# Kernel optimization log

Hardware: AMD Instinct MI355X
Metric: run time of the kernel (lower is better)

## Reference

```python
import jax, jax.numpy as jnp
import numpy as np

T, NC, NT, D, H, LBL = 8, 512, 512, 256, 8, 3
NBF = 1419  # performer default: int(256 * ln(256))
EPS = 1e-4


def setup_inputs() -> dict:
    key = jax.random.key(0)
    ks = jax.random.split(key, 16)
    rn = lambda i, shape, sc=1.0: jax.random.normal(ks[i], shape, dtype=jnp.float32) * sc
    w = 1.0 / np.sqrt(D)
    return {
        'x_ctx': rn(0, (T, NC, D)),
        'label_train': rn(1, (T, NC, LBL)),
        'x_tgt': rn(2, (T, NT, D)),
        # task_encoder: 3-layer MLP (256+label_dim -> 256 -> 256 -> 256), ReLU
        'W1': rn(3, (D + LBL, D), 1.0 / np.sqrt(D + LBL)), 'b1': jnp.zeros((D,), jnp.float32),
        'W2': rn(4, (D, D), w), 'b2': jnp.zeros((D,), jnp.float32),
        'W3': rn(5, (D, D), w), 'b3': jnp.zeros((D,), jnp.float32),
        # per-head projections (8 distinct 256->256 Linears each for k/v/q)
        'Wk': rn(6, (H, D, D), w), 'bk': jnp.zeros((H, D), jnp.float32),
        'Wv': rn(7, (H, D, D), w), 'bv': jnp.zeros((H, D), jnp.float32),
        'Wq': rn(8, (H, D, D), w), 'bq': jnp.zeros((H, D), jnp.float32),
        # output head-merge projection (8*256 -> 256) and mu (256 -> 256)
        'Wo': rn(9, (H * D, D), 1.0 / np.sqrt(H * D)), 'bo': jnp.zeros((D,), jnp.float32),
        'Wmu': rn(10, (D, D), w), 'bmu': jnp.zeros((D,), jnp.float32),
        # FAVOR+ random projection matrix [nb_features, dim_head]
        'proj': rn(11, (NBF, D)),
    }


def _softmax_kernel(data, proj, is_query):
    # Performer FAVOR+ positive softmax-kernel features. data: [t,h,n,d]
    dn = D ** -0.25
    ratio = NBF ** -0.5
    dd = jnp.einsum('thnd,fd->thnf', data * dn, proj)          # [t,h,n,F]
    diag = 0.5 * jnp.sum(data * data, axis=-1) * (dn * dn)      # [t,h,n]
    if is_query:
        m = jnp.max(dd, axis=-1, keepdims=True)
    else:
        m = jnp.max(dd, axis=(-2, -1), keepdims=True)
    return ratio * (jnp.exp(dd - diag[..., None] - m) + EPS)


def reference(x_ctx, label_train, x_tgt, W1, b1, W2, b2, W3, b3,
              Wk, bk, Wv, bv, Wq, bq, Wo, bo, Wmu, bmu, proj):
    # task_encoder MLP on [x_ctx, label]
    h = jax.nn.relu(jnp.concatenate([x_ctx, label_train], axis=-1) @ W1 + b1)
    h = jax.nn.relu(h @ W2 + b2)
    cf = jax.nn.relu(h @ W3 + b3)                               # context_features [t,Nc,D]
    # per-head full-width projections: k from x_ctx, v from context_features, q from x_tgt
    k = jnp.einsum('tnd,hde->thne', x_ctx, Wk) + bk[None, :, None, :]
    v = jnp.einsum('tnd,hde->thne', cf, Wv) + bv[None, :, None, :]
    q = jnp.einsum('tnd,hde->thne', x_tgt, Wq) + bq[None, :, None, :]
    # non-causal Performer linear attention
    qp = _softmax_kernel(q, proj, True)                         # [t,h,Nt,F]
    kp = _softmax_kernel(k, proj, False)                        # [t,h,Nc,F]
    ksum = jnp.sum(kp, axis=-2)                                 # [t,h,F]
    d_inv = 1.0 / jnp.einsum('thnf,thf->thn', qp, ksum)         # [t,h,Nt]
    ctx = jnp.einsum('thnf,thne->thfe', kp, v)                  # [t,h,F,D]
    out = jnp.einsum('thnf,thfe,thn->thne', qp, ctx, d_inv)     # [t,h,Nt,D]
    # torch: permute(0,2,3,1).view(t,Nt,-1) -> head index fastest-varying
    out = jnp.transpose(out, (0, 2, 3, 1)).reshape(out.shape[0], out.shape[2], -1)
    rep = out @ Wo + bo                                         # [t,Nt,D]
    return rep @ Wmu + bmu                                      # mu / sample_features
```

## Files before the change

### kernel.cpp

```cpp
#include <hip/hip_runtime.h>
#include <hip/hip_bf16.h>

typedef __hip_bfloat16 bf16;
typedef __attribute__((ext_vector_type(8))) short short8;
typedef __attribute__((ext_vector_type(4))) float f32x4;
typedef __attribute__((ext_vector_type(4))) unsigned short us4;
#define DEV __device__ __forceinline__

static constexpr int T_ = 8, NC = 512, NT = 512, D_ = 256, H_ = 8, NBF = 1419;
static constexpr int FT32 = 46;
static constexpr float EPS_ = 1e-4f;
static constexpr float DN = 0.25f;
static constexpr float DIAG_SC = 0.03125f;

DEV float bf2f(unsigned short u) { return __uint_as_float(((unsigned)u) << 16); }
DEV float tofloat(bf16 x) { return __bfloat162float(x); }
DEV unsigned short f2bu(float x) { bf16 h = __float2bfloat16(x); return *(unsigned short*)&h; }

DEV float ldx(const void* p, long i, int isb) {
  if (isb) return bf2f(((const unsigned short*)p)[i]);
  return ((const float*)p)[i];
}
DEV void stx(void* p, long i, float v, int isb) {
  if (isb) ((bf16*)p)[i] = __float2bfloat16(v);
  else     ((float*)p)[i] = v;
}
DEV void unpack8(uint4 u, float* dst) {
  unsigned w[4] = {u.x, u.y, u.z, u.w};
#pragma unroll
  for (int i = 0; i < 4; i++) {
    dst[2 * i + 0] = __uint_as_float((w[i] & 0xffffu) << 16);
    dst[2 * i + 1] = __uint_as_float(w[i] & 0xffff0000u);
  }
}

DEV void async_copy16(const void* g, void* lds) {
  __builtin_amdgcn_global_load_lds(
      (const __attribute__((address_space(1))) unsigned int*)g,
      (__attribute__((address_space(3))) unsigned int*)lds, 16, 0, 0);
}

__global__ __launch_bounds__(256)
void detect_dtype(const void* __restrict__ x, int* __restrict__ flag)
{
  __shared__ int bad;
  if (threadIdx.x == 0) bad = 0;
  __syncthreads();
  int mybad = 0;
  for (int j = 0; j < 16; j++) {
    long i = 2L * (threadIdx.x + 256L * j);
    unsigned short u = ((const unsigned short*)x)[i];
    int e = (u >> 7) & 0xff, mant = u & 0x7f;
    bool b = (e == 0xff) || (e >= 141) || (e <= 93 && !(e == 0 && mant == 0));
    mybad += b ? 1 : 0;
  }
  atomicAdd(&bad, mybad);
  __syncthreads();
  if (threadIdx.x == 0) *flag = (bad > 1024) ? 0 : 1;
}

__global__ __launch_bounds__(256)
void conv_proj(const void* __restrict__ proj, bf16* __restrict__ projB,
               const int* __restrict__ dtFlag)
{
  const int fl = *dtFlag;
  int f = blockIdx.x, t = threadIdx.x;
  float v = (f < NBF) ? ldx(proj, (long)f * 256 + t, fl) : 0.f;
  projB[(long)f * 256 + t] = __float2bfloat16(v);
}

__global__ __launch_bounds__(256)
void conv_bf16(const void* __restrict__ src, bf16* __restrict__ dst,
               const int* __restrict__ dtFlag)
{
  const int fl = *dtFlag;
  long i = (long)blockIdx.x * 256 + threadIdx.x;
  dst[i] = __float2bfloat16(ldx(src, i, fl));
}

__global__ __launch_bounds__(256)
void conv_wT(const void* __restrict__ Wk, const void* __restrict__ Wv,
             const void* __restrict__ Wq, const void* __restrict__ Wo,
             const void* __restrict__ W1, const void* __restrict__ W2,
             const void* __restrict__ W3, const void* __restrict__ Wmu,
             bf16* __restrict__ WkT, bf16* __restrict__ WvT,
             bf16* __restrict__ WqT, bf16* __restrict__ WoT,
             bf16* __restrict__ W1T, bf16* __restrict__ W2T,
             bf16* __restrict__ W3T, bf16* __restrict__ WmuT,
             const int* __restrict__ dtFlag)
{
  __shared__ float tile[32][33];
  const int fl = *dtFlag;
  const int kt = blockIdx.x, nt = blockIdx.y, z = blockIdx.z, t = threadIdx.x;
  const void* in; bf16* out; int K; int perm = 0; long off = 0;
  if (z < 8)        { in = Wk;  out = WkT;  K = 256; off = (long)z * 65536; }
  else if (z < 16)  { in = Wv;  out = WvT;  K = 256; off = (long)(z - 8) * 65536; }
  else if (z < 24)  { in = Wq;  out = WqT;  K = 256; off = (long)(z - 16) * 65536; }
  else if (z == 24) { in = Wo;  out = WoT;  K = 2048; perm = 1; }
  else if (z == 25) { in = W1;  out = W1T;  K = 256; }
  else if (z == 26) { in = W2;  out = W2T;  K = 256; }
  else if (z == 27) { in = W3;  out = W3T;  K = 256; }
  else              { in = Wmu; out = WmuT; K = 256; }
  if (K == 256 && kt >= 8) return;
  const int k0 = kt * 32, n0 = nt * 32;
  const int row = t >> 3, cb = (t & 7) * 4;
  {
    int kk = k0 + row;
    int krow = perm ? (((kk & 255) << 3) | (kk >> 8)) : kk;
#pragma unroll
    for (int j = 0; j < 4; j++)
      tile[row][cb + j] = ldx(in, off + (long)krow * 256 + n0 + cb + j, fl);
  }
  __syncthreads();
  us4 o;
#pragma unroll
  for (int j = 0; j < 4; j++) o[j] = f2bu(tile[cb + j][row]);
  *(us4*)(out + off + (long)(n0 + row) * K + k0 + cb) = o;
}

__global__ __launch_bounds__(256)
void init_zero(float* __restrict__ p)
{
  p[blockIdx.x * 256 + threadIdx.x] = 0.f;
}

__global__ __launch_bounds__(256)
void gemm_mfma(const bf16* __restrict__ A, const bf16* __restrict__ BT,
               const void* __restrict__ bias,
               void* __restrict__ C, int cMode, int epi, int cT,
               const int* __restrict__ dtFlag, float* __restrict__ diagOut,
               float* __restrict__ svOut,
               int M, int N, int K, long sA, int divA, long sB, int modB, long sBias)
{
  __shared__ alignas(16) bf16 As[2][64 * 64];
  __shared__ alignas(16) bf16 Bs[2][64 * 64];
  const int fl = *dtFlag;
  const int cB = (cMode == 2) ? fl : cMode;
  const int t = threadIdx.x;
  const int bz = blockIdx.z;
  const long aOff = (long)(bz / divA) * sA;
  const long bOff = (long)(bz % modB) * sB;
  const long biasOff = (long)(bz % modB) * sBias;
  const long cOff = (long)bz * (long)M * N;
  const int m0 = blockIdx.y * 64, n0 = blockIdx.x * 64;
  const int w = t >> 6, l = t & 63, quad = l >> 4, ln = l & 15;
  const bf16* Ab = A + aOff + (long)m0 * K;
  const bf16* Bb = BT + bOff + (long)n0 * K;
  const int srow = l >> 3;
  const int scc = (l & 7) ^ srow;
  f32x4 acc[4] = {};

  auto stage = [&](int buf, int k0) {
#pragma unroll
    for (int j = 0; j < 2; j++) {
      const int rbase = 32 * j + 8 * w;
      const int row = rbase + srow;
      async_copy16(Ab + (long)row * K + k0 + scc * 8, &As[buf][rbase * 64]);
      async_copy16(Bb + (long)row * K + k0 + scc * 8, &Bs[buf][rbase * 64]);
    }
  };

  stage(0, 0);
  __syncthreads();

  int cur = 0;
  for (int k0 = 0; k0 < K; k0 += 64) {
    if (k0 + 64 < K) stage(cur ^ 1, k0 + 64);
    const bf16* Ac = &As[cur][0];
    const bf16* Bc = &Bs[cur][0];
    const int arow = 16 * w + ln;
#pragma unroll
    for (int ks = 0; ks < 2; ks++) {
      short8 a = *(const short8*)(Ac + arow * 64 + (((ks * 4 + quad) ^ (arow & 7)) << 3));
#pragma unroll
      for (int i = 0; i < 4; i++) {
        const int brow = 16 * i + ln;
        short8 b = *(const short8*)(Bc + brow * 64 + (((ks * 4 + quad) ^ (brow & 7)) << 3));
        acc[i] = __builtin_amdgcn_mfma_f32_16x16x32_bf16(a, b, acc[i], 0, 0, 0);
      }
    }
    asm volatile("s_waitcnt vmcnt(0)" ::: "memory");
    __builtin_amdgcn_s_barrier();
    __builtin_amdgcn_sched_barrier(0);
    cur ^= 1;
  }

  float s2[4] = {0.f, 0.f, 0.f, 0.f};
  if (cT == 2) {
    const int mm = m0 + 16 * w + quad * 4;
    const int tile = mm >> 5, off = mm & 31;
#pragma unroll
    for (int i = 0; i < 4; i++) {
      int n = n0 + 16 * i + ln;
      us4 cv;
      float colsum = 0.f;
#pragma unroll
      for (int r = 0; r < 4; r++) {
        float c = acc[i][r];
        if (epi >= 1) c += ldx(bias, biasOff + n, fl);
        if (epi == 2) c = fmaxf(c, 0.f);
        colsum += c;
        cv[r] = f2bu(c);
      }
      *(us4*)((bf16*)C + cOff + ((long)tile * N + n) * 32 + off) = cv;
      if (svOut) {
        colsum += __shfl_xor(colsum, 16);
        colsum += __shfl_xor(colsum, 32);
        if (quad == 0) atomicAdd(&svOut[(long)bz * N + n], colsum);
      }
    }
  } else {
#pragma unroll
    for (int i = 0; i < 4; i++) {
#pragma unroll
      for (int r = 0; r < 4; r++) {
        int m = m0 + 16 * w + quad * 4 + r;
        int n = n0 + 16 * i + ln;
        float c = acc[i][r];
        if (epi >= 1) c += ldx(bias, biasOff + n, fl);
        if (epi == 2) c = fmaxf(c, 0.f);
        s2[r] += c * c;
        stx(C, cOff + (long)m * N + n, c, cB);
      }
    }
  }
  if (diagOut) {
#pragma unroll
    for (int r = 0; r < 4; r++) {
      float s = s2[r];
      s += __shfl_xor(s, 1); s += __shfl_xor(s, 2);
      s += __shfl_xor(s, 4); s += __shfl_xor(s, 8);
      if (ln == 0)
        atomicAdd(&diagOut[(long)bz * M + m0 + 16 * w + quad * 4 + r], DIAG_SC * s);
    }
  }
}

__global__ __launch_bounds__(256)
void gemm_wo_splitk(const bf16* __restrict__ A, const bf16* __restrict__ BT,
                    float* __restrict__ P, int M, int N, int K)
{
  __shared__ alignas(16) bf16 As[2][64 * 64];
  __shared__ alignas(16) bf16 Bs[2][64 * 64];
  const int t = threadIdx.x;
  const int z = blockIdx.z;
  const int m0 = blockIdx.y * 64, n0 = blockIdx.x * 64;
  const int w = t >> 6, l = t & 63, quad = l >> 4, ln = l & 15;
  const bf16* Ab = A + (long)m0 * K;
  const bf16* Bb = BT + (long)n0 * K;
  const int srow = l >> 3, scc = (l & 7) ^ srow;
  f32x4 acc[4] = {};
  const int kbase = z * 256, kend = kbase + 256;

  auto stage = [&](int buf, int k0) {
#pragma unroll
    for (int j = 0; j < 2; j++) {
      const int rbase = 32 * j + 8 * w;
      const int row = rbase + srow;
      async_copy16(Ab + (long)row * K + k0 + scc * 8, &As[buf][rbase * 64]);
      async_copy16(Bb + (long)row * K + k0 + scc * 8, &Bs[buf][rbase * 64]);
    }
  };

  stage(0, kbase);
  __syncthreads();

  int cur = 0;
  for (int k0 = kbase; k0 < kend; k0 += 64) {
    if (k0 + 64 < kend) stage(cur ^ 1, k0 + 64);
    const bf16* Ac = &As[cur][0];
    const bf16* Bc = &Bs[cur][0];
    const int arow = 16 * w + ln;
#pragma unroll
    for (int ks = 0; ks < 2; ks++) {
      short8 a = *(const short8*)(Ac + arow * 64 + (((ks * 4 + quad) ^ (arow & 7)) << 3));
#pragma unroll
      for (int i = 0; i < 4; i++) {
        const int brow = 16 * i + ln;
        short8 b = *(const short8*)(Bc + brow * 64 + (((ks * 4 + quad) ^ (brow & 7)) << 3));
        acc[i] = __builtin_amdgcn_mfma_f32_16x16x32_bf16(a, b, acc[i], 0, 0, 0);
      }
    }
    asm volatile("s_waitcnt vmcnt(0)" ::: "memory");
    __builtin_amdgcn_s_barrier();
    __builtin_amdgcn_sched_barrier(0);
    cur ^= 1;
  }

  float* Pz = P + (long)z * M * N;
#pragma unroll
  for (int i = 0; i < 4; i++) {
#pragma unroll
    for (int r = 0; r < 4; r++) {
      int m = m0 + 16 * w + quad * 4 + r;
      int n = n0 + 16 * i + ln;
      Pz[(long)m * N + n] = acc[i][r];
    }
  }
}

__global__ __launch_bounds__(256)
void reduce_partials(const float* __restrict__ P, const void* __restrict__ bo,
                     bf16* __restrict__ rep, const int* __restrict__ dtFlag)
{
  const int fl = *dtFlag;
  long idx = (long)blockIdx.x * 256 + threadIdx.x;
  int n = idx & 255;
  float s = ldx(bo, n, fl);
#pragma unroll
  for (int z = 0; z < 8; z++) s += P[(long)z * 1048576 + idx];
  rep[idx] = __float2bfloat16(s);
}

__global__ __launch_bounds__(256)
void fixup_h1(bf16* __restrict__ h1, const void* __restrict__ label,
              const void* __restrict__ W1, const void* __restrict__ b1,
              const int* __restrict__ dtFlag)
{
  const int fl = *dtFlag;
  int idx = blockIdx.x * 256 + threadIdx.x;
  int m = idx >> 8, n = idx & 255;
  float c = tofloat(h1[idx]) + ldx(b1, n, fl);
#pragma unroll
  for (int j = 0; j < 3; j++)
    c += ldx(label, m * 3 + j, fl) * ldx(W1, (256 + j) * 256 + n, fl);
  h1[idx] = __float2bfloat16(fmaxf(c, 0.f));
}

__global__ __launch_bounds__(256)
void key_fused_mfma(const bf16* __restrict__ k, const bf16* __restrict__ vQ,
                    const bf16* __restrict__ projB, const float* __restrict__ diagk,
                    float* __restrict__ ksumE, bf16* __restrict__ ctxQ,
                    float* __restrict__ mpart)
{
  __shared__ alignas(16) bf16 kS[3][32 * 256];
  __shared__ alignas(16) bf16 pS[2][64 * 40];
  __shared__ float wredM[4];

  const int bz = blockIdx.x, ft = blockIdx.y, f0 = ft * 64;
  const int t = threadIdx.x;
  const int w = t >> 6, l = t & 63, quad = l >> 4, ln = l & 15;
  const int fmine = f0 + 16 * w + ln;
  const bool fv = fmine < NBF;

  const bf16* kb = k + (long)bz * NC * 256;
  const bf16* vqb = vQ + (long)bz * 16 * 256 * 32;
  const float* db = diagk + bz * NC;

  auto stage = [&](int buf, int n0) {
#pragma unroll
    for (int j = 0; j < 4; j++) {
      int row = w * 8 + j * 2 + (l >> 5);
      int cc = (l & 31) ^ ((2 * j + (l >> 5)) & 7);
      async_copy16(kb + (long)(n0 + row) * 256 + cc * 8,
                   &kS[buf][w * 2048 + j * 512]);
    }
  };
  stage(0, 0);
  stage(1, 32);

  short8 pf[8];
  {
    const bf16* prow = projB + (long)fmine * 256;
#pragma unroll
    for (int kc = 0; kc < 8; kc++)
      pf[kc] = *(const short8*)(prow + kc * 32 + quad * 8);
  }

  f32x4 acc[4][4] = {};
  float ksumP = 0.f, mP = -1e30f;

  __syncthreads();

  int cur = 0;
  for (int it = 0; it < 16; it++) {
    const int n0 = it * 32;
    short8 bfr[4];
#pragma unroll
    for (int ei = 0; ei < 4; ei++) {
      int e = 64 * w + 16 * ei + ln;
      bfr[ei] = *(const short8*)(vqb + ((long)it * 256 + e) * 32 + quad * 8);
    }
    f32x4 dv0 = *(const f32x4*)(db + n0 + quad * 4);
    f32x4 dv1 = *(const f32x4*)(db + n0 + 16 + quad * 4);
    __builtin_amdgcn_sched_barrier(0);
    if (it + 2 < 16) {
      int nb = cur + 2; if (nb >= 3) nb -= 3;
      stage(nb, n0 + 64);
    }
    __builtin_amdgcn_sched_barrier(0);

    const bf16* kcur = &kS[cur][0];
    f32x4 dd[2][2] = {};
    __builtin_amdgcn_s_setprio(1);
#pragma unroll
    for (int kc = 0; kc < 8; kc++) {
      const int hf = kc & 1;
#pragma unroll
      for (int mi = 0; mi < 2; mi++) {
        short8 a = *(const short8*)(kcur + (16 * mi + ln) * 256 +
                                    (((kc * 4 + quad) ^ (ln & 7)) << 3));
        dd[mi][hf] = __builtin_amdgcn_mfma_f32_16x16x32_bf16(a, pf[kc], dd[mi][hf], 0, 0, 0);
      }
    }
    __builtin_amdgcn_s_setprio(0);
    bf16* pcur = &pS[it & 1][0];
#pragma unroll
    for (int mi = 0; mi < 2; mi++) {
      us4 ev;
      f32x4 dvv = mi ? dv1 : dv0;
#pragma unroll
      for (int r = 0; r < 4; r++) {
        float sc = DN * (dd[mi][0][r] + dd[mi][1][r]);
        float E = fv ? __expf(fminf(sc - dvv[r], 80.f)) : 0.f;
        unsigned short u = f2bu(E);
        ksumP += bf2f(u);
        if (fv) mP = fmaxf(mP, sc);
        ev[r] = u;
      }
      *(us4*)(pcur + (16 * w + ln) * 40 + 16 * mi + quad * 4) = ev;
    }
    asm volatile("s_waitcnt vmcnt(4) lgkmcnt(0)" ::: "memory");
    __builtin_amdgcn_s_barrier();
    __builtin_amdgcn_sched_barrier(0);

    __builtin_amdgcn_s_setprio(1);
#pragma unroll
    for (int fh = 0; fh < 4; fh++) {
      short8 a = *(const short8*)(pcur + (16 * fh + ln) * 40 + quad * 8);
#pragma unroll
      for (int ei = 0; ei < 4; ei++)
        acc[fh][ei] = __builtin_amdgcn_mfma_f32_16x16x32_bf16(a, bfr[ei], acc[fh][ei], 0, 0, 0);
    }
    __builtin_amdgcn_s_setprio(0);
    cur = (cur == 2) ? 0 : cur + 1;
  }
  __syncthreads();

#pragma unroll
  for (int fh = 0; fh < 4; fh++) {
    const int ft32 = 2 * ft + (fh >> 1);
    const int f32b = 16 * (fh & 1) + quad * 4;
#pragma unroll
    for (int ei = 0; ei < 4; ei++) {
      int e = 64 * w + 16 * ei + ln;
      us4 cv;
#pragma unroll
      for (int r = 0; r < 4; r++) cv[r] = f2bu(acc[fh][ei][r]);
      *(us4*)(&ctxQ[((long)(bz * FT32 + ft32) * 256 + e) * 32 + f32b]) = cv;
    }
  }

  float s = ksumP;
  s += __shfl_xor(s, 16); s += __shfl_xor(s, 32);
  if (quad == 0 && fv) ksumE[(long)bz * NBF + fmine] = s;
  float m = mP;
#pragma unroll
  for (int off = 1; off < 64; off <<= 1) m = fmaxf(m, __shfl_xor(m, off));
  if (l == 0) wredM[w] = m;
  __syncthreads();
  if (t == 0)
    mpart[bz * 23 + ft] = fmaxf(fmaxf(wredM[0], wredM[1]), fmaxf(wredM[2], wredM[3]));
}

__global__ __launch_bounds__(64)
void mk_reduce(const float* __restrict__ mpart, float* __restrict__ mk)
{
  int bz = blockIdx.x, l = threadIdx.x;
  float m = (l < 23) ? mpart[bz * 23 + l] : -1e30f;
#pragma unroll
  for (int off = 32; off > 0; off >>= 1) m = fmaxf(m, __shfl_down(m, off));
  if (l == 0) mk[bz] = m;
}

__global__ __launch_bounds__(256)
void ctx_finQ(bf16* __restrict__ ctxQ, const float* __restrict__ Sv,
              const float* __restrict__ mk, float* __restrict__ ctxs)
{
  int ft32 = blockIdx.x, bz = blockIdx.y, e = threadIdx.x;
  float emk = __expf(-mk[bz]);
  float sve = EPS_ * Sv[bz * 256 + e];
  uint4* row = (uint4*)(ctxQ + ((long)(bz * FT32 + ft32) * 256 + e) * 32);
  int fbase = 32 * ft32;
  float rsum = 0.f;
#pragma unroll
  for (int cchunk = 0; cchunk < 4; cchunk++) {
    float tmp[8];
    unpack8(row[cchunk], tmp);
    unsigned short out[8];
#pragma unroll
    for (int j = 0; j < 8; j++) {
      int f = fbase + cchunk * 8 + j;
      float val = (f < NBF) ? (emk * tmp[j] + sve) : 0.f;
      rsum += val;
      out[j] = f2bu(val);
    }
    row[cchunk] = *(const uint4*)out;
  }
  atomicAdd(&ctxs[bz * 256 + e], rsum);
}

__global__ __launch_bounds__(256)
void ksum_fin(float* __restrict__ ksumE, const float* __restrict__ mk,
              float* __restrict__ ksumtot)
{
  __shared__ float red[4];
  int bz = blockIdx.x, t = threadIdx.x;
  int f = blockIdx.y * 256 + t;
  float emk = __expf(-mk[bz]);
  float s = 0.f;
  if (f < NBF) {
    float kf = emk * ksumE[(long)bz * NBF + f] + (float)NC * EPS_;
    ksumE[(long)bz * NBF + f] = kf;
    s = kf;
  }
#pragma unroll
  for (int off = 32; off > 0; off >>= 1) s += __shfl_down(s, off);
  if ((t & 63) == 0) red[t >> 6] = s;
  __syncthreads();
  if (t == 0) atomicAdd(&ksumtot[bz], red[0] + red[1] + red[2] + red[3]);
}

__global__ __launch_bounds__(256)
void q_fused_mfma(const bf16* __restrict__ q, const bf16* __restrict__ projB,
                  const float* __restrict__ diagq, const bf16* __restrict__ ctxQ,
                  const float* __restrict__ ksum, const float* __restrict__ ctxsum,
                  const float* __restrict__ ksumtot, bf16* __restrict__ merged)
{
  __shared__ alignas(16) bf16 projS[2][32 * 256];
  __shared__ alignas(16) bf16 eS[64 * 40];
  __shared__ float dS[64];
  __shared__ float csS[256];
  __shared__ float sS[64];
  __shared__ float mS[64];

  const int bz = blockIdx.x, nt = blockIdx.y, t = threadIdx.x;
  const int w = t >> 6, l = t & 63, quad = l >> 4, ln = l & 15;
  const int tq = bz / H_, hh = bz % H_;
  const bf16* cqb = ctxQ + (long)bz * FT32 * 256 * 32;
  const bf16* qb = q + ((long)bz * NT + nt * 64) * 256;

  auto stage_proj = [&](int buf, int f0n) {
#pragma unroll
    for (int j = 0; j < 4; j++) {
      int row = 8 * w + 2 * j + (l >> 5);
      int cc = (l & 31) ^ (row & 7);
      async_copy16(projB + (long)(f0n + row) * 256 + cc * 8,
                   &projS[buf][(8 * w + 2 * j) * 256]);
    }
  };
  stage_proj(0, 0);

  short8 qf[8];
  {
    const bf16* qrow = qb + (long)(16 * w + ln) * 256;
#pragma unroll
    for (int kc = 0; kc < 8; kc++)
      qf[kc] = *(const short8*)(qrow + kc * 32 + quad * 8);
  }
  if (t < 64) dS[t] = diagq[(long)bz * NT + nt * 64 + t];
  csS[t] = ctxsum[bz * 256 + t];

  f32x4 acc[4][4] = {};
  float sPart[4] = {0.f, 0.f, 0.f, 0.f};
  float mPart[4] = {0.f, 0.f, 0.f, 0.f};
  __syncthreads();

  for (int ft = 0; ft < FT32; ft++) {
    const int f0 = ft * 32;
    const bf16* pcur = &projS[ft & 1][0];
    short8 cfr[4];
#pragma unroll
    for (int i = 0; i < 4; i++) {
      int e = 16 * (4 * w + i) + ln;
      cfr[i] = *(const short8*)(cqb + ((long)ft * 256 + e) * 32 + quad * 8);
    }
    const float kv0 = (f0 + ln < NBF) ? ksum[(long)bz * NBF + f0 + ln] : 0.f;
    const float kv1 = (f0 + 16 + ln < NBF) ? ksum[(long)bz * NBF + f0 + 16 + ln] : 0.f;
    if (ft + 1 < FT32) stage_proj((ft + 1) & 1, f0 + 32);

    f32x4 dd0 = {}, dd1 = {};
#pragma unroll
    for (int kc = 0; kc < 8; kc++) {
      const int co = ((kc * 4 + quad) ^ (ln & 7)) << 3;
      short8 b0 = *(const short8*)(pcur + ln * 256 + co);
      dd0 = __builtin_amdgcn_mfma_f32_16x16x32_bf16(qf[kc], b0, dd0, 0, 0, 0);
      short8 b1 = *(const short8*)(pcur + (16 + ln) * 256 + co);
      dd1 = __builtin_amdgcn_mfma_f32_16x16x32_bf16(qf[kc], b1, dd1, 0, 0, 0);
    }
    const bool fv0 = (f0 + ln) < NBF;
    const bool fv1 = (f0 + 16 + ln) < NBF;
#pragma unroll
    for (int r = 0; r < 4; r++) {
      float E0 = fv0 ? __expf(fminf(DN * dd0[r], 80.f)) : 0.f;
      float E1 = fv1 ? __expf(fminf(DN * dd1[r], 80.f)) : 0.f;
      bf16 h0 = __float2bfloat16(E0), h1v = __float2bfloat16(E1);
      float e0 = tofloat(h0), e1 = tofloat(h1v);
      eS[(16 * w + quad * 4 + r) * 40 + ln] = h0;
      eS[(16 * w + quad * 4 + r) * 40 + 16 + ln] = h1v;
      sPart[r] += e0 * kv0 + e1 * kv1;
      mPart[r] = fmaxf(mPart[r], fmaxf(e0, e1));
    }
    asm volatile("s_waitcnt lgkmcnt(0)" ::: "memory");
    __builtin_amdgcn_s_barrier();
    __builtin_amdgcn_sched_barrier(0);

#pragma unroll
    for (int mh = 0; mh < 4; mh++) {
      short8 a = *(const short8*)(&eS[(16 * mh + ln) * 40 + quad * 8]);
#pragma unroll
      for (int i = 0; i < 4; i++)
        acc[mh][i] = __builtin_amdgcn_mfma_f32_16x16x32_bf16(a, cfr[i], acc[mh][i], 0, 0, 0);
    }
    asm volatile("s_waitcnt vmcnt(0) lgkmcnt(0)" ::: "memory");
    __builtin_amdgcn_s_barrier();
    __builtin_amdgcn_sched_barrier(0);
  }
  __syncthreads();

#pragma unroll
  for (int r = 0; r < 4; r++) {
    float s = sPart[r], m = mPart[r];
#pragma unroll
    for (int off = 1; off < 16; off <<= 1) {
      s += __shfl_xor(s, off);
      m = fmaxf(m, __shfl_xor(m, off));
    }
    if (ln == 0) {
      sS[16 * w + quad * 4 + r] = s;
      mS[16 * w + quad * 4 + r] = m;
    }
  }
  __syncthreads();

  const float ktotv = ksumtot[bz];
#pragma unroll
  for (int mh = 0; mh < 4; mh++) {
#pragma unroll
    for (int r = 0; r < 4; r++) {
      int row = 16 * mh + quad * 4 + r;
      float st = sS[row];
      float mt = fmaxf(mS[row], 1e-30f);
      float c = __expf(-dS[row]) / mt;
      float inv = 1.f / (c * st + EPS_ * ktotv);
#pragma unroll
      for (int i = 0; i < 4; i++) {
        int e = 16 * (4 * w + i) + ln;
        float val = (c * acc[mh][i][r] + EPS_ * csS[e]) * inv;
        merged[((long)tq * NT + nt * 64 + row) * 2048 + hh * 256 + e] =
            __float2bfloat16(val);
      }
    }
  }
}

extern "C" void kernel_launch(void* const* d_in, const int* in_sizes, int n_in,
                              void* d_out, int out_size, void* d_ws, size_t ws_size,
                              hipStream_t stream)
{
  const void* x_ctx = d_in[0];
  const void* label = d_in[1];
  const void* x_tgt = d_in[2];
  const void* W1 = d_in[3];
  const void* b1 = d_in[4];
  const void* W2 = d_in[5];
  const void* b2 = d_in[6];
  const void* W3 = d_in[7];
  const void* b3 = d_in[8];
  const void* Wk = d_in[9];
  const void* bk = d_in[10];
  const void* Wv = d_in[11];
  const void* bv = d_in[12];
  const void* Wq = d_in[13];
  const void* bq = d_in[14];
  const void* Wo = d_in[15];
  const void* bo = d_in[16];
  const void* Wmu = d_in[17];
  const void* bmu = d_in[18];
  const void* proj = d_in[19];

  float* W = (float*)d_ws;
  const long F0 = 0, F1 = 4194304, F2 = 8388608;
  const long CTXQ_F = (long)64 * FT32 * 256 * 32 / 2;
  const long F3 = F2 + CTXQ_F;
  bf16* kB = (bf16*)(W + F0);
  bf16* qB = (bf16*)(W + F0);
  bf16* rep = (bf16*)(W + F0);
  bf16* vQ = (bf16*)(W + F1);
  bf16* merged = (bf16*)(W + F1);
  bf16* xtB = (bf16*)(W + F1);
  bf16* h1 = (bf16*)(W + F2);
  bf16* h2 = (bf16*)(W + F2 + 524288);
  bf16* cf = (bf16*)(W + F2 + 1048576);
  bf16* xcB = (bf16*)(W + F2 + 1572864);
  bf16* ctxQ = (bf16*)(W + F2);
  float* woP = W + F2;
  long o = F3;
  auto alloc = [&](long n) { float* p = W + o; o += n; return p; };
  float* zbase = W + o;
  float* dgk = alloc(32768);
  float* dgq = alloc(32768);
  float* Sv = alloc(64 * 256);
  float* ctxs = alloc(64 * 256);
  float* ktot = alloc(64);
  alloc(192);
  float* ksumE = alloc((long)64 * NBF);
  float* mpart = alloc(64 * 23);
  float* mk = alloc(64);
  int* dtFlag = (int*)alloc(64);
  bf16* projB = (bf16*)alloc((long)FT32 * 32 * 256 / 2);
  bf16* WkT = (bf16*)alloc(262144);
  bf16* WvT = (bf16*)alloc(262144);
  bf16* WqT = (bf16*)alloc(262144);
  bf16* WoT = (bf16*)alloc(262144);
  bf16* W1T = (bf16*)alloc(32768);
  bf16* W2T = (bf16*)alloc(32768);
  bf16* W3T = (bf16*)alloc(32768);
  bf16* WmuT = (bf16*)alloc(32768);
  (void)ws_size; (void)in_sizes; (void)n_in; (void)out_size;

  const dim3 B(256);
  detect_dtype<<<1, B, 0, stream>>>(x_ctx, dtFlag);
  conv_proj<<<FT32 * 32, B, 0, stream>>>(proj, projB, dtFlag);
  conv_wT<<<dim3(64, 8, 29), B, 0, stream>>>(Wk, Wv, Wq, Wo, W1, W2, W3, Wmu,
                                             WkT, WvT, WqT, WoT, W1T, W2T, W3T, WmuT, dtFlag);
  conv_bf16<<<4096, B, 0, stream>>>(x_ctx, xcB, dtFlag);
  init_zero<<<385, B, 0, stream>>>(zbase);
  gemm_mfma<<<dim3(4, 64, 1), B, 0, stream>>>(
      xcB, W1T, nullptr, h1, 1, 0, 0, dtFlag, nullptr, nullptr,
      4096, 256, 256, 0L, 1, 0L, 1, 0L);
  fixup_h1<<<4096, B, 0, stream>>>(h1, label, W1, b1, dtFlag);
  gemm_mfma<<<dim3(4, 64, 1), B, 0, stream>>>(
      h1, W2T, b2, h2, 1, 2, 0, dtFlag, nullptr, nullptr,
      4096, 256, 256, 0L, 1, 0L, 1, 0L);
  gemm_mfma<<<dim3(4, 64, 1), B, 0, stream>>>(
      h2, W3T, b3, cf, 1, 2, 0, dtFlag, nullptr, nullptr,
      4096, 256, 256, 0L, 1, 0L, 1, 0L);
  gemm_mfma<<<dim3(4, 8, 64), B, 0, stream>>>(
      xcB, WkT, bk, kB, 1, 1, 0, dtFlag, dgk, nullptr,
      512, 256, 256, 131072L, 8, 65536L, 8, 256L);
  gemm_mfma<<<dim3(4, 8, 64), B, 0, stream>>>(
      cf, WvT, bv, vQ, 1, 1, 2, dtFlag, nullptr, Sv,
      512, 256, 256, 131072L, 8, 65536L, 8, 256L);
  key_fused_mfma<<<dim3(64, 23), B, 0, stream>>>(kB, vQ, projB, dgk, ksumE, ctxQ, mpart);
  mk_reduce<<<64, 64, 0, stream>>>(mpart, mk);
  ctx_finQ<<<dim3(FT32, 64), B, 0, stream>>>(ctxQ, Sv, mk, ctxs);
  ksum_fin<<<dim3(64, 6), B, 0, stream>>>(ksumE, mk, ktot);
  conv_bf16<<<4096, B, 0, stream>>>(x_tgt, xtB, dtFlag);
  gemm_mfma<<<dim3(4, 8, 64), B, 0, stream>>>(
      xtB, WqT, bq, qB, 1, 1, 0, dtFlag, dgq, nullptr,
      512, 256, 256, 131072L, 8, 65536L, 8, 256L);
  q_fused_mfma<<<dim3(64, 8), B, 0, stream>>>(qB, projB, dgq, ctxQ, ksumE, ctxs, ktot, merged);
  gemm_wo_splitk<<<dim3(4, 64, 8), B, 0, stream>>>(merged, WoT, woP, 4096, 256, 2048);
  reduce_partials<<<4096, B, 0, stream>>>(woP, bo, rep, dtFlag);
  gemm_mfma<<<dim3(4, 64, 1), B, 0, stream>>>(
      rep, WmuT, bmu, d_out, 2, 1, 0, dtFlag, nullptr, nullptr,
      4096, 256, 256, 0L, 1, 0L, 1, 0L);
}
```

Baseline: 425.1 us.

## Fold key-side max/eps normalization into query kernel; drop ctx_finQ and ksum_fin

The key kernel now also accumulates raw column sums of ctx and the total ksum via atomics. The query kernel applies the exp(-mk) scaling and the EPS terms algebraically in its epilogue, which removes the ctx_finQ and ksum_fin passes that re-read and re-wrote ctxQ and ksumE. It also cuts Wo split-K from 8 to 2 partial slices, so the reduction reads less. In exchange the key kernel's K staging goes from triple to double buffering with a full vmcnt(0) wait, which may expose load latency. The query kernel now reads an un-rescaled ksumE, which relies on the algebra matching exactly.

```diff
diff --git a/kernel.cpp b/kernel.cpp
--- a/kernel.cpp
+++ b/kernel.cpp
@@ -24,14 +24,6 @@
 DEV void stx(void* p, long i, float v, int isb) {
   if (isb) ((bf16*)p)[i] = __float2bfloat16(v);
   else     ((float*)p)[i] = v;
-}
-DEV void unpack8(uint4 u, float* dst) {
-  unsigned w[4] = {u.x, u.y, u.z, u.w};
-#pragma unroll
-  for (int i = 0; i < 4; i++) {
-    dst[2 * i + 0] = __uint_as_float((w[i] & 0xffffu) << 16);
-    dst[2 * i + 1] = __uint_as_float(w[i] & 0xffff0000u);
-  }
 }
 
 DEV void async_copy16(const void* g, void* lds) {
@@ -250,7 +242,7 @@
   const bf16* Bb = BT + (long)n0 * K;
   const int srow = l >> 3, scc = (l & 7) ^ srow;
   f32x4 acc[4] = {};
-  const int kbase = z * 256, kend = kbase + 256;
+  const int kbase = z * 1024, kend = kbase + 1024;
 
   auto stage = [&](int buf, int k0) {
 #pragma unroll
@@ -306,9 +298,7 @@
   const int fl = *dtFlag;
   long idx = (long)blockIdx.x * 256 + threadIdx.x;
   int n = idx & 255;
-  float s = ldx(bo, n, fl);
-#pragma unroll
-  for (int z = 0; z < 8; z++) s += P[(long)z * 1048576 + idx];
+  float s = ldx(bo, n, fl) + P[idx] + P[1048576 + idx];
   rep[idx] = __float2bfloat16(s);
 }
 
@@ -331,9 +321,10 @@
 void key_fused_mfma(const bf16* __restrict__ k, const bf16* __restrict__ vQ,
                     const bf16* __restrict__ projB, const float* __restrict__ diagk,
                     float* __restrict__ ksumE, bf16* __restrict__ ctxQ,
-                    float* __restrict__ mpart)
-{
-  __shared__ alignas(16) bf16 kS[3][32 * 256];
+                    float* __restrict__ mpart, float* __restrict__ csR,
+                    float* __restrict__ ktotR)
+{
+  __shared__ alignas(16) bf16 kS[2][32 * 256];
   __shared__ alignas(16) bf16 pS[2][64 * 40];
   __shared__ float wredM[4];
 
@@ -357,7 +348,6 @@
     }
   };
   stage(0, 0);
-  stage(1, 32);
 
   short8 pf[8];
   {
@@ -384,10 +374,7 @@
     f32x4 dv0 = *(const f32x4*)(db + n0 + quad * 4);
     f32x4 dv1 = *(const f32x4*)(db + n0 + 16 + quad * 4);
     __builtin_amdgcn_sched_barrier(0);
-    if (it + 2 < 16) {
-      int nb = cur + 2; if (nb >= 3) nb -= 3;
-      stage(nb, n0 + 64);
-    }
+    if (it + 1 < 16) stage(cur ^ 1, n0 + 32);
     __builtin_amdgcn_sched_barrier(0);
 
     const bf16* kcur = &kS[cur][0];
@@ -420,7 +407,7 @@
       }
       *(us4*)(pcur + (16 * w + ln) * 40 + 16 * mi + quad * 4) = ev;
     }
-    asm volatile("s_waitcnt vmcnt(4) lgkmcnt(0)" ::: "memory");
+    asm volatile("s_waitcnt vmcnt(0) lgkmcnt(0)" ::: "memory");
     __builtin_amdgcn_s_barrier();
     __builtin_amdgcn_sched_barrier(0);
 
@@ -433,7 +420,7 @@
         acc[fh][ei] = __builtin_amdgcn_mfma_f32_16x16x32_bf16(a, bfr[ei], acc[fh][ei], 0, 0, 0);
     }
     __builtin_amdgcn_s_setprio(0);
-    cur = (cur == 2) ? 0 : cur + 1;
+    cur ^= 1;
   }
   __syncthreads();
 
@@ -451,9 +438,26 @@
     }
   }
 
+#pragma unroll
+  for (int ei = 0; ei < 4; ei++) {
+    float col = 0.f;
+#pragma unroll
+    for (int fh = 0; fh < 4; fh++)
+#pragma unroll
+      for (int r = 0; r < 4; r++) col += acc[fh][ei][r];
+    col += __shfl_xor(col, 16);
+    col += __shfl_xor(col, 32);
+    if (quad == 0) atomicAdd(&csR[(long)bz * 256 + 64 * w + 16 * ei + ln], col);
+  }
+
   float s = ksumP;
   s += __shfl_xor(s, 16); s += __shfl_xor(s, 32);
   if (quad == 0 && fv) ksumE[(long)bz * NBF + fmine] = s;
+  float s2 = s;
+  s2 += __shfl_xor(s2, 1); s2 += __shfl_xor(s2, 2);
+  s2 += __shfl_xor(s2, 4); s2 += __shfl_xor(s2, 8);
+  if (l == 0) atomicAdd(&ktotR[bz], s2);
+
   float m = mP;
 #pragma unroll
   for (int off = 1; off < 64; off <<= 1) m = fmaxf(m, __shfl_xor(m, off));
@@ -474,71 +478,27 @@
 }
 
 __global__ __launch_bounds__(256)
-void ctx_finQ(bf16* __restrict__ ctxQ, const float* __restrict__ Sv,
-              const float* __restrict__ mk, float* __restrict__ ctxs)
-{
-  int ft32 = blockIdx.x, bz = blockIdx.y, e = threadIdx.x;
-  float emk = __expf(-mk[bz]);
-  float sve = EPS_ * Sv[bz * 256 + e];
-  uint4* row = (uint4*)(ctxQ + ((long)(bz * FT32 + ft32) * 256 + e) * 32);
-  int fbase = 32 * ft32;
-  float rsum = 0.f;
-#pragma unroll
-  for (int cchunk = 0; cchunk < 4; cchunk++) {
-    float tmp[8];
-    unpack8(row[cchunk], tmp);
-    unsigned short out[8];
-#pragma unroll
-    for (int j = 0; j < 8; j++) {
-      int f = fbase + cchunk * 8 + j;
-      float val = (f < NBF) ? (emk * tmp[j] + sve) : 0.f;
-      rsum += val;
-      out[j] = f2bu(val);
-    }
-    row[cchunk] = *(const uint4*)out;
-  }
-  atomicAdd(&ctxs[bz * 256 + e], rsum);
-}
-
-__global__ __launch_bounds__(256)
-void ksum_fin(float* __restrict__ ksumE, const float* __restrict__ mk,
-              float* __restrict__ ksumtot)
-{
-  __shared__ float red[4];
-  int bz = blockIdx.x, t = threadIdx.x;
-  int f = blockIdx.y * 256 + t;
-  float emk = __expf(-mk[bz]);
-  float s = 0.f;
-  if (f < NBF) {
-    float kf = emk * ksumE[(long)bz * NBF + f] + (float)NC * EPS_;
-    ksumE[(long)bz * NBF + f] = kf;
-    s = kf;
-  }
-#pragma unroll
-  for (int off = 32; off > 0; off >>= 1) s += __shfl_down(s, off);
-  if ((t & 63) == 0) red[t >> 6] = s;
-  __syncthreads();
-  if (t == 0) atomicAdd(&ksumtot[bz], red[0] + red[1] + red[2] + red[3]);
-}
-
-__global__ __launch_bounds__(256)
 void q_fused_mfma(const bf16* __restrict__ q, const bf16* __restrict__ projB,
                   const float* __restrict__ diagq, const bf16* __restrict__ ctxQ,
-                  const float* __restrict__ ksum, const float* __restrict__ ctxsum,
-                  const float* __restrict__ ksumtot, bf16* __restrict__ merged)
+                  const float* __restrict__ ksum, const float* __restrict__ Sv,
+                  const float* __restrict__ csR, const float* __restrict__ ktotR,
+                  const float* __restrict__ mk, bf16* __restrict__ merged)
 {
   __shared__ alignas(16) bf16 projS[2][32 * 256];
   __shared__ alignas(16) bf16 eS[64 * 40];
   __shared__ float dS[64];
-  __shared__ float csS[256];
+  __shared__ float svS[256];
+  __shared__ float crS[256];
   __shared__ float sS[64];
   __shared__ float mS[64];
+  __shared__ float seS[64];
 
   const int bz = blockIdx.x, nt = blockIdx.y, t = threadIdx.x;
   const int w = t >> 6, l = t & 63, quad = l >> 4, ln = l & 15;
   const int tq = bz / H_, hh = bz % H_;
   const bf16* cqb = ctxQ + (long)bz * FT32 * 256 * 32;
   const bf16* qb = q + ((long)bz * NT + nt * 64) * 256;
+  const float emk = __expf(-mk[bz]);
 
   auto stage_proj = [&](int buf, int f0n) {
 #pragma unroll
@@ -559,10 +519,12 @@
       qf[kc] = *(const short8*)(qrow + kc * 32 + quad * 8);
   }
   if (t < 64) dS[t] = diagq[(long)bz * NT + nt * 64 + t];
-  csS[t] = ctxsum[bz * 256 + t];
+  svS[t] = Sv[bz * 256 + t];
+  crS[t] = csR[bz * 256 + t];
 
   f32x4 acc[4][4] = {};
   float sPart[4] = {0.f, 0.f, 0.f, 0.f};
+  float sEp[4] = {0.f, 0.f, 0.f, 0.f};
   float mPart[4] = {0.f, 0.f, 0.f, 0.f};
   __syncthreads();
 
@@ -599,6 +561,7 @@
       eS[(16 * w + quad * 4 + r) * 40 + ln] = h0;
       eS[(16 * w + quad * 4 + r) * 40 + 16 + ln] = h1v;
       sPart[r] += e0 * kv0 + e1 * kv1;
+      sEp[r] += e0 + e1;
       mPart[r] = fmaxf(mPart[r], fmaxf(e0, e1));
     }
     asm volatile("s_waitcnt lgkmcnt(0)" ::: "memory");
@@ -620,33 +583,38 @@
 
 #pragma unroll
   for (int r = 0; r < 4; r++) {
-    float s = sPart[r], m = mPart[r];
+    float s = sPart[r], m = mPart[r], se = sEp[r];
 #pragma unroll
     for (int off = 1; off < 16; off <<= 1) {
       s += __shfl_xor(s, off);
       m = fmaxf(m, __shfl_xor(m, off));
+      se += __shfl_xor(se, off);
     }
     if (ln == 0) {
       sS[16 * w + quad * 4 + r] = s;
       mS[16 * w + quad * 4 + r] = m;
-    }
-  }
-  __syncthreads();
-
-  const float ktotv = ksumtot[bz];
+      seS[16 * w + quad * 4 + r] = se;
+    }
+  }
+  __syncthreads();
+
+  const float ktotv = ktotR[bz];
 #pragma unroll
   for (int mh = 0; mh < 4; mh++) {
 #pragma unroll
     for (int r = 0; r < 4; r++) {
       int row = 16 * mh + quad * 4 + r;
       float st = sS[row];
+      float se = seS[row];
       float mt = fmaxf(mS[row], 1e-30f);
       float c = __expf(-dS[row]) / mt;
-      float inv = 1.f / (c * st + EPS_ * ktotv);
+      float A = c * se + (float)NBF * EPS_;
+      float den = emk * (c * st + EPS_ * ktotv) + (float)NC * EPS_ * A;
+      float inv = 1.f / den;
 #pragma unroll
       for (int i = 0; i < 4; i++) {
         int e = 16 * (4 * w + i) + ln;
-        float val = (c * acc[mh][i][r] + EPS_ * csS[e]) * inv;
+        float val = (emk * (c * acc[mh][i][r] + EPS_ * crS[e]) + EPS_ * svS[e] * A) * inv;
         merged[((long)tq * NT + nt * 64 + row) * 2048 + hh * 256 + e] =
             __float2bfloat16(val);
       }
@@ -701,8 +669,8 @@
   float* dgk = alloc(32768);
   float* dgq = alloc(32768);
   float* Sv = alloc(64 * 256);
-  float* ctxs = alloc(64 * 256);
-  float* ktot = alloc(64);
+  float* csR = alloc(64 * 256);
+  float* ktotR = alloc(64);
   alloc(192);
   float* ksumE = alloc((long)64 * NBF);
   float* mpart = alloc(64 * 23);
@@ -742,16 +710,16 @@
   gemm_mfma<<<dim3(4, 8, 64), B, 0, stream>>>(
       cf, WvT, bv, vQ, 1, 1, 2, dtFlag, nullptr, Sv,
       512, 256, 256, 131072L, 8, 65536L, 8, 256L);
-  key_fused_mfma<<<dim3(64, 23), B, 0, stream>>>(kB, vQ, projB, dgk, ksumE, ctxQ, mpart);
+  key_fused_mfma<<<dim3(64, 23), B, 0, stream>>>(kB, vQ, projB, dgk, ksumE, ctxQ,
+                                                 mpart, csR, ktotR);
   mk_reduce<<<64, 64, 0, stream>>>(mpart, mk);
-  ctx_finQ<<<dim3(FT32, 64), B, 0, stream>>>(ctxQ, Sv, mk, ctxs);
-  ksum_fin<<<dim3(64, 6), B, 0, stream>>>(ksumE, mk, ktot);
   conv_bf16<<<4096, B, 0, stream>>>(x_tgt, xtB, dtFlag);
   gemm_mfma<<<dim3(4, 8, 64), B, 0, stream>>>(
       xtB, WqT, bq, qB, 1, 1, 0, dtFlag, dgq, nullptr,
       512, 256, 256, 131072L, 8, 65536L, 8, 256L);
-  q_fused_mfma<<<dim3(64, 8), B, 0, stream>>>(qB, projB, dgq, ctxQ, ksumE, ctxs, ktot, merged);
-  gemm_wo_splitk<<<dim3(4, 64, 8), B, 0, stream>>>(merged, WoT, woP, 4096, 256, 2048);
+  q_fused_mfma<<<dim3(64, 8), B, 0, stream>>>(qB, projB, dgq, ctxQ, ksumE,
+                                              Sv, csR, ktotR, mk, merged);
+  gemm_wo_splitk<<<dim3(4, 64, 2), B, 0, stream>>>(merged, WoT, woP, 4096, 256, 2048);
   reduce_partials<<<4096, B, 0, stream>>>(woP, bo, rep, dtFlag);
   gemm_mfma<<<dim3(4, 64, 1), B, 0, stream>>>(
       rep, WmuT, bmu, d_out, 2, 1, 0, dtFlag, nullptr, nullptr,
```

Measured after the change: 417.9 us. No clear change (-1.7%).
